# Kernel optimization log

Hardware: AMD Instinct MI355X
Metric: run time of the kernel (lower is better)

The kernel has to match this reference:

```python
import jax, jax.numpy as jnp
import numpy as np

B, S, N_IN, N_OUT = 4, 192, 256, 1

def setup_inputs() -> dict:
    key = jax.random.key(0)
    ks = jax.random.split(key, 7)
    scale = 1.0 / np.sqrt(N_IN)
    return {
        "h_head": jax.random.normal(ks[0], (B, S, N_IN), jnp.float32),
        "h_dep": jax.random.normal(ks[1], (B, S, N_IN), jnp.float32),
        "h_sib": jax.random.normal(ks[2], (B, S, N_IN), jnp.float32),
        "W_tri": jax.random.normal(ks[3], (N_OUT, N_IN, N_IN, N_IN), jnp.float32) * (scale / N_IN),
        "U_hd": jax.random.normal(ks[4], (N_OUT, N_IN, N_IN), jnp.float32) * scale,
        "V_hs": jax.random.normal(ks[5], (N_OUT, N_IN, N_IN), jnp.float32) * scale,
        "Z_ds": jax.random.normal(ks[6], (N_OUT, N_IN, N_IN), jnp.float32) * scale,
        "bias": jnp.zeros((N_OUT,), jnp.float32),
    }

def reference(h_head, h_dep, h_sib, W_tri, U_hd, V_hs, Z_ds, bias):
    # biaffine terms: [b, x, y, o]
    s_hd = jnp.einsum('bhi,oij,bdj->bhdo', h_head, U_hd, h_dep)
    s_hs = jnp.einsum('bhi,oij,bsj->bhso', h_head, V_hs, h_sib)
    s_ds = jnp.einsum('bdi,oij,bsj->bdso', h_dep, Z_ds, h_sib)
    # trilinear term: note j,k of W_tri appear nowhere else, so they are
    # reduced first (w_red[o,i] = sum_{j,k} W_tri[o,i,j,k]) — same math as
    # torch.einsum('bhi,bdi,bsi,oijk->bhdso', ...).
    w_red = jnp.sum(W_tri, axis=(2, 3))  # [o, i]
    s_tri = jnp.einsum('bhi,bdi,bsi,oi->bhdso', h_head, h_dep, h_sib, w_red)
    scores = (s_tri
              + s_hd[:, :, :, None, :]   # unsqueeze sib axis
              + s_hs[:, :, None, :, :]   # unsqueeze dep axis
              + s_ds[:, None, :, :, :]   # unsqueeze head axis
              + bias)
    return scores[..., 0]  # n_out == 1 -> squeeze last dim
```

## Files before the change

### kernel.cpp

```cpp
#include <hip/hip_runtime.h>
#include <stdint.h>

#define NB 4
#define SS 192
#define NI 256

typedef __attribute__((ext_vector_type(8))) short bf16x8;
typedef __attribute__((ext_vector_type(16))) float f32x16;

__device__ __forceinline__ uint16_t f2bf(float f) {
  union { float f; uint32_t u; } v; v.f = f;
  return (uint16_t)((v.u + 0x7FFFu + ((v.u >> 16) & 1u)) >> 16);
}

__device__ __forceinline__ uint4 pack8(const float4 a, const float4 b) {
  uint4 r;
  r.x = (uint32_t)f2bf(a.x) | ((uint32_t)f2bf(a.y) << 16);
  r.y = (uint32_t)f2bf(a.z) | ((uint32_t)f2bf(a.w) << 16);
  r.z = (uint32_t)f2bf(b.x) | ((uint32_t)f2bf(b.y) << 16);
  r.w = (uint32_t)f2bf(b.z) | ((uint32_t)f2bf(b.w) << 16);
  return r;
}

__device__ __forceinline__ uint32_t bfmul2(uint32_t x, uint32_t y) {
  union { float f; uint32_t u; } xa, xb, ya, yb, r0, r1;
  xa.u = x << 16;        ya.u = y << 16;
  xb.u = x & 0xFFFF0000u; yb.u = y & 0xFFFF0000u;
  r0.f = xa.f * ya.f;
  r1.f = xb.f * yb.f;
  uint32_t lo = (r0.u + 0x7FFFu + ((r0.u >> 16) & 1u)) >> 16;
  uint32_t hi = (r1.u + 0x7FFFu + ((r1.u >> 16) & 1u)) >> 16;
  return lo | (hi << 16);
}


__global__ __launch_bounds__(256) void k0(
    const float* __restrict__ W,
    const float* __restrict__ h_head, const float* __restrict__ h_dep, const float* __restrict__ h_sib,
    const float* __restrict__ U, const float* __restrict__ V, const float* __restrict__ Z,
    float* __restrict__ partial,
    uint16_t* __restrict__ HH, uint16_t* __restrict__ HD, uint16_t* __restrict__ HS,
    uint16_t* __restrict__ U16, uint16_t* __restrict__ V16, uint16_t* __restrict__ Z16) {
  __shared__ float red[4];
  const int bi = blockIdx.x, tid = threadIdx.x;
  if (bi < 2048) {
    const float4* pw = (const float4*)(W + (size_t)bi * 8192);
    float4 a = {0.f, 0.f, 0.f, 0.f};
    #pragma unroll
    for (int it = 0; it < 8; ++it) {
      const float4 v = pw[it * 256 + tid];
      a.x += v.x; a.y += v.y; a.z += v.z; a.w += v.w;
    }
    float s = (a.x + a.y) + (a.z + a.w);
    for (int off = 32; off > 0; off >>= 1) s += __shfl_down(s, off, 64);
    if ((tid & 63) == 0) red[tid >> 6] = s;
    __syncthreads();
    if (tid == 0) partial[bi] = red[0] + red[1] + red[2] + red[3];
    return;
  }
  const int rl = tid >> 5, c8 = tid & 31;
  if (bi < 2144) {
    const int g = (bi - 2048) * 8 + rl;
    const int dst = g * 32 + (c8 ^ (g & 15));
    const int srci = g * 64 + c8 * 2;
    { const float4 x = ((const float4*)h_head)[srci], y = ((const float4*)h_head)[srci + 1];
      ((uint4*)HH)[dst] = pack8(x, y); }
    { const float4 x = ((const float4*)h_dep)[srci], y = ((const float4*)h_dep)[srci + 1];
      ((uint4*)HD)[dst] = pack8(x, y); }
    { const float4 x = ((const float4*)h_sib)[srci], y = ((const float4*)h_sib)[srci + 1];
      ((uint4*)HS)[dst] = pack8(x, y); }
  } else {
    const int g = (bi - 2144) * 8 + rl;
    const int dst = g * 32 + (c8 ^ (g & 15));
    const int srci = g * 64 + c8 * 2;
    { const float4 x = ((const float4*)U)[srci], y = ((const float4*)U)[srci + 1];
      ((uint4*)U16)[dst] = pack8(x, y); }
    { const float4 x = ((const float4*)V)[srci], y = ((const float4*)V)[srci + 1];
      ((uint4*)V16)[dst] = pack8(x, y); }
    { const float4 x = ((const float4*)Z)[srci], y = ((const float4*)Z)[srci + 1];
      ((uint4*)Z16)[dst] = pack8(x, y); }
  }
}

__global__ __launch_bounds__(256, 2) void k_s1(
    const uint16_t* __restrict__ HD, const uint16_t* __restrict__ HS,
    const uint16_t* __restrict__ U16, const uint16_t* __restrict__ V16, const uint16_t* __restrict__ Z16,
    uint16_t* __restrict__ dU16, uint16_t* __restrict__ T216, uint16_t* __restrict__ TZ16) {
  __shared__ __align__(16) uint16_t Ah[192 * 128];
  __shared__ __align__(16) uint16_t Bh[128 * 128];
  const int which = blockIdx.x, nt = blockIdx.y, b = blockIdx.z;
  const uint16_t* As = (which == 0) ? HD : HS;
  const uint16_t* Bs = (which == 0) ? U16 : (which == 1) ? V16 : Z16;
  uint16_t* Os = (which == 0) ? dU16 : (which == 1) ? T216 : TZ16;
  const int tid = threadIdx.x, lane = tid & 63, w = tid >> 6;
  const int l31 = lane & 31, l5 = lane >> 5;
  const int N0 = nt * 128;
  f32x16 acc[6] = {};

  #pragma unroll
  for (int kh = 0; kh < 2; ++kh) {
    const int kbase = kh * 128;
    if (kh) __syncthreads();
    #pragma unroll
    for (int i = 0; i < 12; ++i) {
      const int slot = i * 256 + tid;
      const int row = slot >> 4, ck = slot & 15;
      const uint16_t* src = As + (size_t)(b * SS + row) * NI + kbase + ck * 8;
      __builtin_amdgcn_global_load_lds((const __attribute__((address_space(1))) void*)src,
          (__attribute__((address_space(3))) void*)(Ah + (size_t)slot * 8), 16, 0, 0);
    }
    #pragma unroll
    for (int i = 0; i < 8; ++i) {
      const int slot = i * 256 + tid;
      const int row = slot >> 4, ck = slot & 15;
      const uint16_t* src = Bs + (size_t)(N0 + row) * NI + kbase + ck * 8;
      __builtin_amdgcn_global_load_lds((const __attribute__((address_space(1))) void*)src,
          (__attribute__((address_space(3))) void*)(Bh + (size_t)slot * 8), 16, 0, 0);
    }
    __syncthreads();
    const int brow = w * 32 + l31;
    const int bbyte = brow * 256;
    const int bmask = brow & 15;
    #pragma unroll
    for (int ks = 0; ks < 8; ++ks) {
      const int sl = ks * 2 + l5;
      bf16x8 bf = *reinterpret_cast<const bf16x8*>((const char*)Bh + bbyte + ((sl ^ bmask) << 4));
      #pragma unroll
      for (int mt = 0; mt < 6; ++mt) {
        const int ar = mt * 32 + l31;
        bf16x8 af = *reinterpret_cast<const bf16x8*>((const char*)Ah + ar * 256 + ((sl ^ (ar & 15)) << 4));
        acc[mt] = __builtin_amdgcn_mfma_f32_32x32x16_bf16(af, bf, acc[mt], 0, 0, 0);
      }
    }
  }
  const int n = N0 + w * 32 + l31;
  const int nck = n >> 3, npos = n & 7;
  #pragma unroll
  for (int mt = 0; mt < 6; ++mt) {
    #pragma unroll
    for (int r = 0; r < 16; ++r) {
      const int m = mt * 32 + (r & 3) + 8 * (r >> 2) + 4 * l5;
      Os[(size_t)(b * SS + m) * NI + ((nck ^ (m & 15)) << 3) + npos] = f2bf(acc[mt][r]);
    }
  }
}

__global__ __launch_bounds__(384, 1) void k_s2(
    const uint16_t* __restrict__ HH, const uint16_t* __restrict__ HD,
    const uint16_t* __restrict__ dU16, const uint16_t* __restrict__ T216, const uint16_t* __restrict__ TZ16,
    float* __restrict__ s_hd, float* __restrict__ s_hs, float* __restrict__ s_ds) {
  __shared__ __align__(16) uint16_t Ah[192 * 128];
  __shared__ __align__(16) uint16_t Bh[192 * 128];
  const int which = blockIdx.x, b = blockIdx.y;
  const uint16_t* As = (which == 2) ? HD : HH;
  const uint16_t* Bs = (which == 0) ? dU16 : (which == 1) ? T216 : TZ16;
  float* Os = (which == 0) ? s_hd : (which == 1) ? s_hs : s_ds;
  const int tid = threadIdx.x, lane = tid & 63, w = tid >> 6;
  const int l31 = lane & 31, l5 = lane >> 5;
  f32x16 acc[6] = {};

  #pragma unroll
  for (int kh = 0; kh < 2; ++kh) {
    const int kbase = kh * 128;
    if (kh) __syncthreads();
    #pragma unroll
    for (int i = 0; i < 8; ++i) {
      const int slot = i * 384 + tid;
      const int row = slot >> 4, ck = slot & 15;
      const uint16_t* src = As + (size_t)(b * SS + row) * NI + kbase + ck * 8;
      __builtin_amdgcn_global_load_lds((const __attribute__((address_space(1))) void*)src,
          (__attribute__((address_space(3))) void*)(Ah + (size_t)slot * 8), 16, 0, 0);
    }
    #pragma unroll
    for (int i = 0; i < 8; ++i) {
      const int slot = i * 384 + tid;
      const int row = slot >> 4, ck = slot & 15;
      const uint16_t* src = Bs + (size_t)(b * SS + row) * NI + kbase + ck * 8;
      __builtin_amdgcn_global_load_lds((const __attribute__((address_space(1))) void*)src,
          (__attribute__((address_space(3))) void*)(Bh + (size_t)slot * 8), 16, 0, 0);
    }
    __syncthreads();
    const int brow = w * 32 + l31;
    const int bbyte = brow * 256;
    const int bmask = brow & 15;
    #pragma unroll
    for (int ks = 0; ks < 8; ++ks) {
      const int sl = ks * 2 + l5;
      bf16x8 bf = *reinterpret_cast<const bf16x8*>((const char*)Bh + bbyte + ((sl ^ bmask) << 4));
      #pragma unroll
      for (int mt = 0; mt < 6; ++mt) {
        const int ar = mt * 32 + l31;
        bf16x8 af = *reinterpret_cast<const bf16x8*>((const char*)Ah + ar * 256 + ((sl ^ (ar & 15)) << 4));
        acc[mt] = __builtin_amdgcn_mfma_f32_32x32x16_bf16(af, bf, acc[mt], 0, 0, 0);
      }
    }
  }
  const int n = w * 32 + l31;
  #pragma unroll
  for (int mt = 0; mt < 6; ++mt) {
    #pragma unroll
    for (int r = 0; r < 16; ++r) {
      const int m = mt * 32 + (r & 3) + 8 * (r >> 2) + 4 * l5;
      Os[(size_t)(b * SS + m) * SS + n] = acc[mt][r];
    }
  }
}

__global__ __launch_bounds__(384, 3) void k3_big(
    const uint16_t* __restrict__ HH, const uint16_t* __restrict__ HS,
    const float* __restrict__ h_dep, const float* __restrict__ partial,
    const float* __restrict__ s_hd, const float* __restrict__ s_hs,
    const float* __restrict__ s_ds,
    const float* __restrict__ bias, float* __restrict__ out) {
  __shared__ __align__(16) uint16_t Btile[SS * 128];
  __shared__ __align__(16) uint16_t Atile[96 * 128];
  __shared__ uint16_t cvec[NI];
  const int d = blockIdx.x, hb = blockIdx.y, b = blockIdx.z;
  const int tid = threadIdx.x;
  const int lane = tid & 63, w = tid >> 6;
  const int whb = (w >> 1) * 32;
  const int wsb = (w & 1) * 96;
  const int l31 = lane & 31, l5 = lane >> 5;

  if (tid < NI) {
    float wr = 0.f;
    #pragma unroll
    for (int q = 0; q < 8; ++q) wr += partial[8 * tid + q];
    cvec[tid] = f2bf(wr * h_dep[(b * SS + d) * NI + tid]);
  }
  __syncthreads();

  f32x16 acc0 = {}, acc1 = {}, acc2 = {};

  #pragma unroll
  for (int half = 0; half < 2; ++half) {
    const int kbase = half * 128;
    #pragma unroll
    for (int i = 0; i < 8; ++i) {
      const int slot = (w * 8 + i) * 64 + lane;
      const int row = slot >> 4;
      const uint16_t* src = HS + ((size_t)(b * SS + row) << 8) + kbase + (slot & 15) * 8;
      __builtin_amdgcn_global_load_lds(
          (const __attribute__((address_space(1))) void*)src,
          (__attribute__((address_space(3))) void*)(Btile + (size_t)slot * 8),
          16, 0, 0);
    }
    #pragma unroll
    for (int i = 0; i < 4; ++i) {
      const int c = i * 384 + tid;
      const int row = c >> 4;
      const int kc = c & 15;
      const int lcl = kc ^ (row & 15);
      const uint4 cv4 = *(const uint4*)(cvec + kbase + lcl * 8);
      const uint4 hh4 = *(const uint4*)(HH + ((size_t)(b * SS + hb * 96 + row) << 8) + kbase + kc * 8);
      uint4 a4;
      a4.x = bfmul2(hh4.x, cv4.x);
      a4.y = bfmul2(hh4.y, cv4.y);
      a4.z = bfmul2(hh4.z, cv4.z);
      a4.w = bfmul2(hh4.w, cv4.w);
      *(uint4*)((char*)Atile + row * 256 + (kc << 4)) = a4;
    }
    __syncthreads();
    const int arow = whb + l31;
    const int abyte = arow * 256;
    const int amask = (arow & 15);
    #pragma unroll
    for (int ks = 0; ks < 8; ++ks) {
      const int sl = ks * 2 + l5;
      bf16x8 af = *reinterpret_cast<const bf16x8*>((const char*)Atile + abyte + ((sl ^ amask) << 4));
      {
        const int brow = wsb + l31;
        bf16x8 bf = *reinterpret_cast<const bf16x8*>((const char*)Btile + brow * 256 + ((sl ^ (brow & 15)) << 4));
        acc0 = __builtin_amdgcn_mfma_f32_32x32x16_bf16(af, bf, acc0, 0, 0, 0);
      }
      {
        const int brow = wsb + 32 + l31;
        bf16x8 bf = *reinterpret_cast<const bf16x8*>((const char*)Btile + brow * 256 + ((sl ^ (brow & 15)) << 4));
        acc1 = __builtin_amdgcn_mfma_f32_32x32x16_bf16(af, bf, acc1, 0, 0, 0);
      }
      {
        const int brow = wsb + 64 + l31;
        bf16x8 bf = *reinterpret_cast<const bf16x8*>((const char*)Btile + brow * 256 + ((sl ^ (brow & 15)) << 4));
        acc2 = __builtin_amdgcn_mfma_f32_32x32x16_bf16(af, bf, acc2, 0, 0, 0);
      }
    }
    __syncthreads();
  }

  const float bias0 = bias[0];
  float chd[16];
  #pragma unroll
  for (int r = 0; r < 16; ++r) {
    const int h = hb * 96 + whb + (r & 3) + 8 * (r >> 2) + 4 * l5;
    chd[r] = s_hd[(b * SS + h) * SS + d] + bias0;
  }
  #pragma unroll
  for (int t = 0; t < 3; ++t) {
    const int s = wsb + t * 32 + l31;
    const float dsv = s_ds[(b * SS + d) * SS + s];
    const f32x16 a = (t == 0) ? acc0 : (t == 1) ? acc1 : acc2;
    #pragma unroll
    for (int r = 0; r < 16; ++r) {
      const int h = hb * 96 + whb + (r & 3) + 8 * (r >> 2) + 4 * l5;
      const float v = a[r] + chd[r] + s_hs[(b * SS + h) * SS + s] + dsv;
      out[((size_t)(b * SS + h) * SS + d) * SS + s] = v;
    }
  }
}

extern "C" void kernel_launch(void* const* d_in, const int* in_sizes, int n_in,
                              void* d_out, int out_size, void* d_ws, size_t ws_size,
                              hipStream_t stream) {
  const float* h_head = (const float*)d_in[0];
  const float* h_dep  = (const float*)d_in[1];
  const float* h_sib  = (const float*)d_in[2];
  const float* W_tri  = (const float*)d_in[3];
  const float* U_hd   = (const float*)d_in[4];
  const float* V_hs   = (const float*)d_in[5];
  const float* Z_ds   = (const float*)d_in[6];
  const float* bias   = (const float*)d_in[7];
  float* out = (float*)d_out;

  float* ws = (float*)d_ws;
  float* partial = ws;          ws += 2048;
  float* s_hd    = ws;          ws += NB * SS * SS;
  float* s_hs    = ws;          ws += NB * SS * SS;
  float* s_ds    = ws;          ws += NB * SS * SS;
  uint16_t* HH   = (uint16_t*)ws;
  uint16_t* HD   = HH + NB * SS * NI;
  uint16_t* HS   = HD + NB * SS * NI;
  uint16_t* U16  = HS + NB * SS * NI;
  uint16_t* V16  = U16 + NI * NI;
  uint16_t* Z16  = V16 + NI * NI;
  uint16_t* dU16 = Z16 + NI * NI;
  uint16_t* T216 = dU16 + NB * SS * NI;
  uint16_t* TZ16 = T216 + NB * SS * NI;

  k0<<<2176, 256, 0, stream>>>(W_tri, h_head, h_dep, h_sib, U_hd, V_hs, Z_ds,
                               partial, HH, HD, HS, U16, V16, Z16);
  k_s1<<<dim3(3, 2, NB), 256, 0, stream>>>(HD, HS, U16, V16, Z16, dU16, T216, TZ16);
  k_s2<<<dim3(3, NB), 384, 0, stream>>>(HH, HD, dU16, T216, TZ16, s_hd, s_hs, s_ds);
  k3_big<<<dim3(SS, 2, NB), 384, 0, stream>>>(HH, HS, h_dep, partial,
                                              s_hd, s_hs, s_ds, bias, out);
}
```

Measured before the change: 78.33 us.

## Split k3 sib axis across blocks and use 9 waves with one tile each

The main output kernel now splits the sib dimension into two 96-wide halves across the grid, giving twice as many blocks. Each block runs 9 waves arranged 3x3, and each wave computes a single 32x32 MFMA tile instead of three. This shrinks the B tile in LDS by half and lowers accumulator register pressure, aiming for more parallelism and occupancy. The cost is that every block still builds the full 96-row scaled A tile, so that work is duplicated across sib halves, and the trailing barrier is replaced by a barrier at the start of the second half.

```diff
diff --git a/kernel.cpp b/kernel.cpp
--- a/kernel.cpp
+++ b/kernel.cpp
@@ -206,20 +206,19 @@
   }
 }
 
-__global__ __launch_bounds__(384, 3) void k3_big(
+__global__ __launch_bounds__(576) void k3_big(
     const uint16_t* __restrict__ HH, const uint16_t* __restrict__ HS,
     const float* __restrict__ h_dep, const float* __restrict__ partial,
     const float* __restrict__ s_hd, const float* __restrict__ s_hs,
     const float* __restrict__ s_ds,
     const float* __restrict__ bias, float* __restrict__ out) {
-  __shared__ __align__(16) uint16_t Btile[SS * 128];
+  __shared__ __align__(16) uint16_t Btile[96 * 128];
   __shared__ __align__(16) uint16_t Atile[96 * 128];
   __shared__ uint16_t cvec[NI];
-  const int d = blockIdx.x, hb = blockIdx.y, b = blockIdx.z;
+  const int d = blockIdx.x, hb = blockIdx.y >> 1, sb = blockIdx.y & 1, b = blockIdx.z;
   const int tid = threadIdx.x;
   const int lane = tid & 63, w = tid >> 6;
-  const int whb = (w >> 1) * 32;
-  const int wsb = (w & 1) * 96;
+  const int wh = w / 3, ws = w % 3;
   const int l31 = lane & 31, l5 = lane >> 5;
 
   if (tid < NI) {
@@ -230,81 +229,66 @@
   }
   __syncthreads();
 
-  f32x16 acc0 = {}, acc1 = {}, acc2 = {};
+  f32x16 acc = {};
 
   #pragma unroll
   for (int half = 0; half < 2; ++half) {
     const int kbase = half * 128;
-    #pragma unroll
-    for (int i = 0; i < 8; ++i) {
-      const int slot = (w * 8 + i) * 64 + lane;
-      const int row = slot >> 4;
-      const uint16_t* src = HS + ((size_t)(b * SS + row) << 8) + kbase + (slot & 15) * 8;
-      __builtin_amdgcn_global_load_lds(
-          (const __attribute__((address_space(1))) void*)src,
-          (__attribute__((address_space(3))) void*)(Btile + (size_t)slot * 8),
-          16, 0, 0);
-    }
-    #pragma unroll
-    for (int i = 0; i < 4; ++i) {
-      const int c = i * 384 + tid;
-      const int row = c >> 4;
-      const int kc = c & 15;
-      const int lcl = kc ^ (row & 15);
-      const uint4 cv4 = *(const uint4*)(cvec + kbase + lcl * 8);
-      const uint4 hh4 = *(const uint4*)(HH + ((size_t)(b * SS + hb * 96 + row) << 8) + kbase + kc * 8);
-      uint4 a4;
-      a4.x = bfmul2(hh4.x, cv4.x);
-      a4.y = bfmul2(hh4.y, cv4.y);
-      a4.z = bfmul2(hh4.z, cv4.z);
-      a4.w = bfmul2(hh4.w, cv4.w);
-      *(uint4*)((char*)Atile + row * 256 + (kc << 4)) = a4;
+    if (half) __syncthreads();
+    #pragma unroll
+    for (int i = 0; i < 3; ++i) {
+      const int slot = i * 576 + tid;
+      if (slot < 1536) {
+        const int row = slot >> 4;
+        const uint16_t* src = HS + ((size_t)(b * SS + sb * 96 + row) << 8) + kbase + (slot & 15) * 8;
+        __builtin_amdgcn_global_load_lds(
+            (const __attribute__((address_space(1))) void*)src,
+            (__attribute__((address_space(3))) void*)(Btile + (size_t)slot * 8),
+            16, 0, 0);
+      }
+    }
+    #pragma unroll
+    for (int i = 0; i < 3; ++i) {
+      const int slot = i * 576 + tid;
+      if (slot < 1536) {
+        const int row = slot >> 4;
+        const int kc = slot & 15;
+        const int lcl = kc ^ (row & 15);
+        const uint4 cv4 = *(const uint4*)(cvec + kbase + lcl * 8);
+        const uint4 hh4 = *(const uint4*)(HH + ((size_t)(b * SS + hb * 96 + row) << 8) + kbase + kc * 8);
+        uint4 a4;
+        a4.x = bfmul2(hh4.x, cv4.x);
+        a4.y = bfmul2(hh4.y, cv4.y);
+        a4.z = bfmul2(hh4.z, cv4.z);
+        a4.w = bfmul2(hh4.w, cv4.w);
+        *(uint4*)((char*)Atile + (size_t)slot * 16) = a4;
+      }
     }
     __syncthreads();
-    const int arow = whb + l31;
+    const int arow = wh * 32 + l31;
     const int abyte = arow * 256;
-    const int amask = (arow & 15);
+    const int amask = arow & 15;
+    const int brow = ws * 32 + l31;
+    const int bbyte = brow * 256;
+    const int bmask = brow & 15;
     #pragma unroll
     for (int ks = 0; ks < 8; ++ks) {
       const int sl = ks * 2 + l5;
       bf16x8 af = *reinterpret_cast<const bf16x8*>((const char*)Atile + abyte + ((sl ^ amask) << 4));
-      {
-        const int brow = wsb + l31;
-        bf16x8 bf = *reinterpret_cast<const bf16x8*>((const char*)Btile + brow * 256 + ((sl ^ (brow & 15)) << 4));
-        acc0 = __builtin_amdgcn_mfma_f32_32x32x16_bf16(af, bf, acc0, 0, 0, 0);
-      }
-      {
-        const int brow = wsb + 32 + l31;
-        bf16x8 bf = *reinterpret_cast<const bf16x8*>((const char*)Btile + brow * 256 + ((sl ^ (brow & 15)) << 4));
-        acc1 = __builtin_amdgcn_mfma_f32_32x32x16_bf16(af, bf, acc1, 0, 0, 0);
-      }
-      {
-        const int brow = wsb + 64 + l31;
-        bf16x8 bf = *reinterpret_cast<const bf16x8*>((const char*)Btile + brow * 256 + ((sl ^ (brow & 15)) << 4));
-        acc2 = __builtin_amdgcn_mfma_f32_32x32x16_bf16(af, bf, acc2, 0, 0, 0);
-      }
-    }
-    __syncthreads();
+      bf16x8 bf = *reinterpret_cast<const bf16x8*>((const char*)Btile + bbyte + ((sl ^ bmask) << 4));
+      acc = __builtin_amdgcn_mfma_f32_32x32x16_bf16(af, bf, acc, 0, 0, 0);
+    }
   }
 
   const float bias0 = bias[0];
-  float chd[16];
+  const int s = sb * 96 + ws * 32 + l31;
+  const float dsv = s_ds[(b * SS + d) * SS + s];
   #pragma unroll
   for (int r = 0; r < 16; ++r) {
-    const int h = hb * 96 + whb + (r & 3) + 8 * (r >> 2) + 4 * l5;
-    chd[r] = s_hd[(b * SS + h) * SS + d] + bias0;
-  }
-  #pragma unroll
-  for (int t = 0; t < 3; ++t) {
-    const int s = wsb + t * 32 + l31;
-    const float dsv = s_ds[(b * SS + d) * SS + s];
-    const f32x16 a = (t == 0) ? acc0 : (t == 1) ? acc1 : acc2;
-    #pragma unroll
-    for (int r = 0; r < 16; ++r) {
-      const int h = hb * 96 + whb + (r & 3) + 8 * (r >> 2) + 4 * l5;
-      const float v = a[r] + chd[r] + s_hs[(b * SS + h) * SS + s] + dsv;
-      out[((size_t)(b * SS + h) * SS + d) * SS + s] = v;
-    }
+    const int h = hb * 96 + wh * 32 + (r & 3) + 8 * (r >> 2) + 4 * l5;
+    const float chd = s_hd[(b * SS + h) * SS + d] + bias0;
+    const float v = acc[r] + chd + s_hs[(b * SS + h) * SS + s] + dsv;
+    out[((size_t)(b * SS + h) * SS + d) * SS + s] = v;
   }
 }
 
@@ -340,6 +324,6 @@
                                partial, HH, HD, HS, U16, V16, Z16);
   k_s1<<<dim3(3, 2, NB), 256, 0, stream>>>(HD, HS, U16, V16, Z16, dU16, T216, TZ16);
   k_s2<<<dim3(3, NB), 384, 0, stream>>>(HH, HD, dU16, T216, TZ16, s_hd, s_hs, s_ds);
-  k3_big<<<dim3(SS, 2, NB), 384, 0, stream>>>(HH, HS, h_dep, partial,
+  k3_big<<<dim3(SS, 4, NB), 576, 0, stream>>>(HH, HS, h_dep, partial,
                                               s_hd, s_hs, s_ds, bias, out);
 }
```

After: 78.07 us. No clear change (-0.3%).
